# Kernel optimization log

Hardware: AMD Instinct MI355X
Metric: run time of the kernel (lower is better)

## Reference

```python
import jax, jax.numpy as jnp
import numpy as np

N_NODES = 100_000
N_EDGES = 1_600_000
N_TOKENS = 16
VOCAB = 32_000
TOK_DIM = 64
NODE_DIM = 64
HID = 128
FC = 128
NUM_GRAPHS = 1024


def setup_inputs() -> dict:
    key = jax.random.key(0)
    ks = jax.random.split(key, 14)
    emb = jax.random.normal(ks[0], (VOCAB, TOK_DIM), jnp.float32) * 0.02
    emb = emb.at[0].set(0.0)  # padding_idx=0 row is zero
    return {
        "x_token_idxs": jax.random.randint(ks[1], (N_NODES, N_TOKENS), 0, VOCAB),
        "edge_index": jax.random.randint(ks[2], (2, N_EDGES), 0, N_NODES),
        "batch": jnp.sort(jax.random.randint(ks[3], (N_NODES,), 0, NUM_GRAPHS)),
        "emb": emb,
        "Wp": jax.random.normal(ks[4], (TOK_DIM, NODE_DIM), jnp.float32) * (1.0 / np.sqrt(TOK_DIM)),
        "bp": jnp.zeros((NODE_DIM,), jnp.float32),
        "W1": jax.random.normal(ks[5], (NODE_DIM, HID), jnp.float32) * (1.0 / np.sqrt(NODE_DIM)),
        "b1": jnp.zeros((HID,), jnp.float32),
        "W2": jax.random.normal(ks[6], (HID, HID), jnp.float32) * (1.0 / np.sqrt(HID)),
        "b2": jnp.zeros((HID,), jnp.float32),
        "Wfc": jax.random.normal(ks[7], (HID, FC), jnp.float32) * (1.0 / np.sqrt(HID)),
        "bfc": jnp.zeros((FC,), jnp.float32),
        "Wout": jax.random.normal(ks[8], (FC, 1), jnp.float32) * (1.0 / np.sqrt(FC)),
        "bout": jnp.zeros((1,), jnp.float32),
    }


def reference(x_token_idxs, edge_index, batch, emb, Wp, bp, W1, b1, W2, b2, Wfc, bfc, Wout, bout):
    N = x_token_idxs.shape[0]
    # token embed -> mean pool over tokens -> node projection
    node = emb[x_token_idxs].mean(axis=1) @ Wp + bp  # [N, NODE_DIM]

    # GCN normalization with self-loops (PyG gcn_norm, symmetric)
    loops = jnp.arange(N)
    src = jnp.concatenate([edge_index[0], loops])
    dst = jnp.concatenate([edge_index[1], loops])
    deg = jax.ops.segment_sum(jnp.ones_like(dst, jnp.float32), dst, num_segments=N)
    dis = jnp.where(deg > 0, jax.lax.rsqrt(deg), 0.0)
    norm = (dis[src] * dis[dst])[:, None]  # [E+N, 1]

    def gcn(x, W, b):
        h = x @ W                                      # linear transform first (in->out)
        msg = h[src] * norm                            # gather + scale
        return jax.ops.segment_sum(msg, dst, num_segments=N) + b  # scatter-add + bias

    x = jax.nn.relu(gcn(node, W1, b1))
    x = jax.nn.relu(gcn(x, W2, b2))

    # global mean pool by graph id
    cnt = jax.ops.segment_sum(jnp.ones((N,), jnp.float32), batch, num_segments=NUM_GRAPHS)
    g = jax.ops.segment_sum(x, batch, num_segments=NUM_GRAPHS) / jnp.maximum(cnt, 1.0)[:, None]

    g = jax.nn.relu(g @ Wfc + bfc)
    logits = (g @ Wout + bout).squeeze(-1)  # [NUM_GRAPHS]
    return jax.nn.sigmoid(logits), logits
```

## Files before the change

kernel.cpp:

```cpp
#include <hip/hip_runtime.h>
#include <hip/hip_bf16.h>
#include <hip/hip_fp16.h>
#include <math.h>

#define N_TOKENS 16
#define TOK_DIM 64
#define NODE_DIM 64
#define HID 128
#define FC 128
#define NUM_GRAPHS 1024
#define NBUCK_MAX 512
#define CHUNK 8192

typedef _Float16 f16x8 __attribute__((ext_vector_type(8)));
typedef float f32x4 __attribute__((ext_vector_type(4)));

__device__ __forceinline__ __half2 shfl_xor_h2(__half2 v, int mask) {
    int i = *(int*)&v;
    i = __shfl_xor(i, mask);
    return *(__half2*)&i;
}

__global__ void prep_weights_kernel(const float* __restrict__ Wp, const float* __restrict__ W1,
                                    const float* __restrict__ W2, const float* __restrict__ bp,
                                    _Float16* __restrict__ Wf16t, _Float16* __restrict__ W2t,
                                    float* __restrict__ bf) {
    int n = blockIdx.x;
    int t = threadIdx.x;
    if (t < 64) {
        float acc = 0.f;
#pragma unroll
        for (int d = 0; d < 64; d++) acc += Wp[t * 64 + d] * W1[d * 128 + n];
        Wf16t[(size_t)n * 64 + t] = (_Float16)acc;
    } else {
        int d = t - 64;
        float v = bp[d] * W1[d * 128 + n];
#pragma unroll
        for (int off = 32; off > 0; off >>= 1) v += __shfl_down(v, off);
        if (d == 0) bf[n] = v;
    }
    W2t[(size_t)n * 128 + t] = (_Float16)W2[(size_t)t * 128 + n];
}

__global__ void embed_mean_kernel(const int* __restrict__ tok,
                                  const float* __restrict__ emb,
                                  __half* __restrict__ mean16, int N) {
    int t = threadIdx.x;
    int w = t >> 6, j = t & 63;
    int q = j >> 4, l = j & 15;
    int i = blockIdx.x * 4 + w;
    if (i >= N) return;
    const float4* e4 = (const float4*)emb;
    int t0 = tok[i * 16 + q];
    int t1 = tok[i * 16 + q + 4];
    int t2 = tok[i * 16 + q + 8];
    int t3 = tok[i * 16 + q + 12];
    float4 v0 = e4[(size_t)t0 * 16 + l];
    float4 v1 = e4[(size_t)t1 * 16 + l];
    float4 v2 = e4[(size_t)t2 * 16 + l];
    float4 v3 = e4[(size_t)t3 * 16 + l];
    float4 s;
    s.x = v0.x + v1.x + v2.x + v3.x;
    s.y = v0.y + v1.y + v2.y + v3.y;
    s.z = v0.z + v1.z + v2.z + v3.z;
    s.w = v0.w + v1.w + v2.w + v3.w;
    s.x += __shfl_xor(s.x, 16); s.y += __shfl_xor(s.y, 16);
    s.z += __shfl_xor(s.z, 16); s.w += __shfl_xor(s.w, 16);
    s.x += __shfl_xor(s.x, 32); s.y += __shfl_xor(s.y, 32);
    s.z += __shfl_xor(s.z, 32); s.w += __shfl_xor(s.w, 32);
    if (q == 0) {
        const float inv = 1.0f / 16.0f;
        __half2 h0 = __floats2half2_rn(s.x * inv, s.y * inv);
        __half2 h1 = __floats2half2_rn(s.z * inv, s.w * inv);
        float2 packed;
        ((__half2*)&packed)[0] = h0;
        ((__half2*)&packed)[1] = h1;
        ((float2*)mean16)[(size_t)i * 16 + l] = packed;
    }
}

__global__ void bucket_hist_kernel(const int* __restrict__ dst, int* __restrict__ bucket_cnt,
                                   int E, int nbuck) {
    __shared__ int h[NBUCK_MAX];
    int t = threadIdx.x;
    for (int i = t; i < nbuck; i += 256) h[i] = 0;
    __syncthreads();
    int base = blockIdx.x * CHUNK;
    for (int i = t; i < CHUNK; i += 256) {
        int e = base + i;
        if (e < E) atomicAdd(&h[dst[e] >> 8], 1);
    }
    __syncthreads();
    for (int i = t; i < nbuck; i += 256)
        if (h[i]) atomicAdd(&bucket_cnt[i], h[i]);
}

__global__ void bucket_scan_kernel(const int* __restrict__ bucket_cnt,
                                   int* __restrict__ bucket_base,
                                   int* __restrict__ bucket_cursor, int nbuck) {
    __shared__ int s[512];
    int tid = threadIdx.x;
    int v = (tid < nbuck) ? bucket_cnt[tid] : 0;
    s[tid] = v;
    __syncthreads();
    for (int off = 1; off < 512; off <<= 1) {
        int add = (tid >= off) ? s[tid - off] : 0;
        __syncthreads();
        s[tid] += add;
        __syncthreads();
    }
    if (tid < nbuck) { bucket_base[tid] = s[tid] - v; bucket_cursor[tid] = 0; }
    if (tid == 511) bucket_base[nbuck] = s[511];
}

__global__ void binscatter_kernel(const int* __restrict__ src, const int* __restrict__ dst,
                                  const int* __restrict__ bucket_base,
                                  int* __restrict__ bucket_cursor,
                                  int* __restrict__ staged, int E, int nbuck) {
    __shared__ int h[NBUCK_MAX];
    __shared__ int gw[NBUCK_MAX];
    int t = threadIdx.x;
    for (int i = t; i < nbuck; i += 256) h[i] = 0;
    __syncthreads();
    int base = blockIdx.x * CHUNK;
    for (int i = t; i < CHUNK; i += 256) {
        int e = base + i;
        if (e < E) atomicAdd(&h[dst[e] >> 8], 1);
    }
    __syncthreads();
    for (int i = t; i < nbuck; i += 256) {
        int c = h[i];
        gw[i] = (c > 0) ? bucket_base[i] + atomicAdd(&bucket_cursor[i], c) : 0;
        h[i] = 0;
    }
    __syncthreads();
    for (int i = t; i < CHUNK; i += 256) {
        int e = base + i;
        if (e < E) {
            int d = dst[e], s = src[e];
            int b = d >> 8;
            int r = atomicAdd(&h[b], 1);
            staged[gw[b] + r] = s | ((d & 255) << 17);
        }
    }
}

__global__ void bucket_count_kernel(const int* __restrict__ staged,
                                    const int* __restrict__ bucket_base,
                                    int* __restrict__ row_start, float* __restrict__ dis,
                                    int N, int E) {
    __shared__ int cnt[256];
    __shared__ int sc[256];
    int b = blockIdx.x;
    int t = threadIdx.x;
    cnt[t] = 0;
    __syncthreads();
    int rb0 = bucket_base[b], rb1 = bucket_base[b + 1];
    for (int i = rb0 + t; i < rb1; i += 256) atomicAdd(&cnt[staged[i] >> 17], 1);
    __syncthreads();
    int v = cnt[t];
    sc[t] = v;
    __syncthreads();
    for (int off = 1; off < 256; off <<= 1) {
        int add = (t >= off) ? sc[t - off] : 0;
        __syncthreads();
        sc[t] += add;
        __syncthreads();
    }
    int node = b * 256 + t;
    if (node < N) {
        row_start[node] = rb0 + sc[t] - v;
        dis[node] = rsqrtf(1.0f + (float)v);
    }
    if (b == 0 && t == 0) row_start[N] = E;
}

__global__ void csr_write_kernel(const int* __restrict__ staged,
                                 const int* __restrict__ bucket_base,
                                 const int* __restrict__ row_start,
                                 const float* __restrict__ dis,
                                 int2* __restrict__ csr, float* __restrict__ rowsum, int N) {
    __shared__ int cur[256];
    __shared__ float dl[256];
    __shared__ float wsum[256];
    int b = blockIdx.x;
    int t = threadIdx.x;
    int node = b * 256 + t;
    cur[t] = (node < N) ? row_start[node] : 0;
    dl[t] = (node < N) ? dis[node] : 0.f;
    wsum[t] = 0.f;
    __syncthreads();
    int rb0 = bucket_base[b], rb1 = bucket_base[b + 1];
    for (int i = rb0 + t; i < rb1; i += 256) {
        int v = staged[i];
        int s = v & 131071;
        int dloc = v >> 17;
        float w = dis[s] * dl[dloc];
        int pos = atomicAdd(&cur[dloc], 1);
        __half2 wh = __floats2half2_rn(w, w);
        csr[pos] = make_int2(s, *(int*)&wh);
        atomicAdd(&wsum[dloc], w);
    }
    __syncthreads();
    if (node < N) rowsum[node] = wsum[t] + dl[t] * dl[t];
}

__global__ __launch_bounds__(256, 8)
void agg64_kernel(const __half* __restrict__ mean16,
                  const int* __restrict__ row_start,
                  const int2* __restrict__ csr,
                  const float* __restrict__ dis,
                  __half* __restrict__ agg16, int N) {
    int t = threadIdx.x;
    int w = t >> 6, j = t & 63;
    int q = j >> 3, l = j & 7;
    int node = blockIdx.x * 4 + w;
    if (node >= N) return;
    int beg = row_start[node];
    int end = row_start[node + 1];
    float d = dis[node];
    const float4* m4 = (const float4*)mean16;
    __half2 a0, a1, a2, a3;
    {
        float4 raw = m4[(size_t)node * 8 + l];
        const __half2* hp = (const __half2*)&raw;
        float d2f = d * d * ((q == 0) ? 1.f : 0.f);
        __half2 d2h = __floats2half2_rn(d2f, d2f);
        a0 = __hmul2(hp[0], d2h); a1 = __hmul2(hp[1], d2h);
        a2 = __hmul2(hp[2], d2h); a3 = __hmul2(hp[3], d2h);
    }
    int k = beg;
    int kfull = beg + ((end - beg) & ~31);
    for (; k < kfull; k += 32) {
        int2 e[4];
        float4 v[4];
#pragma unroll
        for (int m = 0; m < 4; m++) e[m] = csr[k + 8 * m + q];
#pragma unroll
        for (int m = 0; m < 4; m++) v[m] = m4[(size_t)e[m].x * 8 + l];
#pragma unroll
        for (int m = 0; m < 4; m++) {
            __half2 wh = *(__half2*)&e[m].y;
            const __half2* hp = (const __half2*)&v[m];
            a0 = __hfma2(hp[0], wh, a0);
            a1 = __hfma2(hp[1], wh, a1);
            a2 = __hfma2(hp[2], wh, a2);
            a3 = __hfma2(hp[3], wh, a3);
        }
    }
    for (; k < end; k += 16) {
        int2 e[2];
        float4 v[2];
#pragma unroll
        for (int m = 0; m < 2; m++) {
            int kk = k + 8 * m + q;
            e[m] = (kk < end) ? csr[kk] : make_int2(0, 0);
        }
#pragma unroll
        for (int m = 0; m < 2; m++) v[m] = m4[(size_t)e[m].x * 8 + l];
#pragma unroll
        for (int m = 0; m < 2; m++) {
            __half2 wh = *(__half2*)&e[m].y;
            const __half2* hp = (const __half2*)&v[m];
            a0 = __hfma2(hp[0], wh, a0);
            a1 = __hfma2(hp[1], wh, a1);
            a2 = __hfma2(hp[2], wh, a2);
            a3 = __hfma2(hp[3], wh, a3);
        }
    }
#pragma unroll
    for (int mask = 8; mask <= 32; mask <<= 1) {
        a0 = __hadd2(a0, shfl_xor_h2(a0, mask));
        a1 = __hadd2(a1, shfl_xor_h2(a1, mask));
        a2 = __hadd2(a2, shfl_xor_h2(a2, mask));
        a3 = __hadd2(a3, shfl_xor_h2(a3, mask));
    }
    if (q == 0) {
        float4 packed;
        __half2* pp = (__half2*)&packed;
        pp[0] = a0; pp[1] = a1; pp[2] = a2; pp[3] = a3;
        ((float4*)agg16)[(size_t)node * 8 + l] = packed;
    }
}

#define NB 32
__global__ void dense_chain_mfma_kernel(const __half* __restrict__ agg16,
                                        const float* __restrict__ rowsum,
                                        const _Float16* __restrict__ Wf16t,
                                        const float* __restrict__ bf,
                                        const float* __restrict__ b1,
                                        const _Float16* __restrict__ W2t,
                                        __half* __restrict__ h2, int N) {
    __shared__ _Float16 sx1[32][136];
    __shared__ float srs[32];
    int t = threadIdx.x;
    int wv = t >> 6, lane = t & 63;
    int nb0 = blockIdx.x * NB;
    int rh = wv & 1;
    int ncb = (wv >> 1) * 64;
    int m16 = lane & 15;
    int q = lane >> 4;

    if (t < 32) srs[t] = (nb0 + t < N) ? rowsum[nb0 + t] : 0.f;

    f32x4 c0 = {}, c1 = {}, c2 = {}, c3 = {};
    int arow = nb0 + rh * 16 + m16;
    bool rowok = (arow < N);
    const _Float16* ag = (const _Float16*)agg16;
#pragma unroll
    for (int ks = 0; ks < 2; ks++) {
        int k0 = ks * 32 + q * 8;
        f16x8 afrag = {};
        if (rowok) afrag = *(const f16x8*)(ag + (size_t)arow * 64 + k0);
        f16x8 b0 = *(const f16x8*)(Wf16t + (size_t)(ncb + 0 * 16 + m16) * 64 + k0);
        f16x8 b1f = *(const f16x8*)(Wf16t + (size_t)(ncb + 1 * 16 + m16) * 64 + k0);
        f16x8 b2f = *(const f16x8*)(Wf16t + (size_t)(ncb + 2 * 16 + m16) * 64 + k0);
        f16x8 b3f = *(const f16x8*)(Wf16t + (size_t)(ncb + 3 * 16 + m16) * 64 + k0);
        c0 = __builtin_amdgcn_mfma_f32_16x16x32_f16(afrag, b0, c0, 0, 0, 0);
        c1 = __builtin_amdgcn_mfma_f32_16x16x32_f16(afrag, b1f, c1, 0, 0, 0);
        c2 = __builtin_amdgcn_mfma_f32_16x16x32_f16(afrag, b2f, c2, 0, 0, 0);
        c3 = __builtin_amdgcn_mfma_f32_16x16x32_f16(afrag, b3f, c3, 0, 0, 0);
    }
    __syncthreads();
    {
        f32x4 cc[4] = {c0, c1, c2, c3};
#pragma unroll
        for (int nt = 0; nt < 4; nt++) {
            int ncol = ncb + nt * 16 + m16;
            float bfj = bf[ncol], b1j = b1[ncol];
#pragma unroll
            for (int r = 0; r < 4; r++) {
                int mrow = q * 4 + r;
                float z = cc[nt][r] + srs[rh * 16 + mrow] * bfj + b1j;
                sx1[rh * 16 + mrow][ncol] = (_Float16)fmaxf(z, 0.f);
            }
        }
    }
    __syncthreads();

    f32x4 d0 = {}, d1 = {}, d2 = {}, d3 = {};
#pragma unroll
    for (int ks = 0; ks < 4; ks++) {
        int k0 = ks * 32 + q * 8;
        f16x8 afrag = *(const f16x8*)(&sx1[rh * 16 + m16][k0]);
        f16x8 b0 = *(const f16x8*)(W2t + (size_t)(ncb + 0 * 16 + m16) * 128 + k0);
        f16x8 b1f = *(const f16x8*)(W2t + (size_t)(ncb + 1 * 16 + m16) * 128 + k0);
        f16x8 b2f = *(const f16x8*)(W2t + (size_t)(ncb + 2 * 16 + m16) * 128 + k0);
        f16x8 b3f = *(const f16x8*)(W2t + (size_t)(ncb + 3 * 16 + m16) * 128 + k0);
        d0 = __builtin_amdgcn_mfma_f32_16x16x32_f16(afrag, b0, d0, 0, 0, 0);
        d1 = __builtin_amdgcn_mfma_f32_16x16x32_f16(afrag, b1f, d1, 0, 0, 0);
        d2 = __builtin_amdgcn_mfma_f32_16x16x32_f16(afrag, b2f, d2, 0, 0, 0);
        d3 = __builtin_amdgcn_mfma_f32_16x16x32_f16(afrag, b3f, d3, 0, 0, 0);
    }
    {
        f32x4 dd[4] = {d0, d1, d2, d3};
#pragma unroll
        for (int nt = 0; nt < 4; nt++) {
            int ncol = ncb + nt * 16 + m16;
#pragma unroll
            for (int r = 0; r < 4; r++) {
                int node = nb0 + rh * 16 + q * 4 + r;
                if (node < N) h2[(size_t)node * 128 + ncol] = __float2half(dd[nt][r]);
            }
        }
    }
}

__global__ __launch_bounds__(256, 8)
void gcn_agg128_kernel(const __half* __restrict__ hsrc,
                       const int* __restrict__ row_start,
                       const int2* __restrict__ csr,
                       const float* __restrict__ dis,
                       const float* __restrict__ b2,
                       __half* __restrict__ outx, int N) {
    int t = threadIdx.x;
    int w = t >> 6, j = t & 63;
    int q = j >> 4, l = j & 15;
    int node = blockIdx.x * 4 + w;
    if (node >= N) return;
    const float4* h4 = (const float4*)hsrc;
    int beg = row_start[node];
    int end = row_start[node + 1];
    float d = dis[node];
    __half2 a0, a1, a2, a3;
    {
        float4 raw = h4[(size_t)node * 16 + l];
        const __half2* hp = (const __half2*)&raw;
        float d2f = d * d * ((q == 0) ? 1.f : 0.f);
        __half2 d2h = __floats2half2_rn(d2f, d2f);
        a0 = __hmul2(hp[0], d2h); a1 = __hmul2(hp[1], d2h);
        a2 = __hmul2(hp[2], d2h); a3 = __hmul2(hp[3], d2h);
    }
    int k = beg;
    int kfull = beg + ((end - beg) & ~31);
    for (; k < kfull; k += 32) {
        int2 e[8];
        float4 v[8];
#pragma unroll
        for (int m = 0; m < 8; m++) e[m] = csr[k + 4 * m + q];
#pragma unroll
        for (int m = 0; m < 8; m++) v[m] = h4[(size_t)e[m].x * 16 + l];
#pragma unroll
        for (int m = 0; m < 8; m++) {
            __half2 wh = *(__half2*)&e[m].y;
            const __half2* hp = (const __half2*)&v[m];
            a0 = __hfma2(hp[0], wh, a0);
            a1 = __hfma2(hp[1], wh, a1);
            a2 = __hfma2(hp[2], wh, a2);
            a3 = __hfma2(hp[3], wh, a3);
        }
    }
    for (; k < end; k += 16) {
        int2 e[4];
        float4 v[4];
#pragma unroll
        for (int m = 0; m < 4; m++) {
            int kk = k + 4 * m + q;
            e[m] = (kk < end) ? csr[kk] : make_int2(0, 0);
        }
#pragma unroll
        for (int m = 0; m < 4; m++) v[m] = h4[(size_t)e[m].x * 16 + l];
#pragma unroll
        for (int m = 0; m < 4; m++) {
            __half2 wh = *(__half2*)&e[m].y;
            const __half2* hp = (const __half2*)&v[m];
            a0 = __hfma2(hp[0], wh, a0);
            a1 = __hfma2(hp[1], wh, a1);
            a2 = __hfma2(hp[2], wh, a2);
            a3 = __hfma2(hp[3], wh, a3);
        }
    }
#pragma unroll
    for (int mask = 16; mask <= 32; mask <<= 1) {
        a0 = __hadd2(a0, shfl_xor_h2(a0, mask));
        a1 = __hadd2(a1, shfl_xor_h2(a1, mask));
        a2 = __hadd2(a2, shfl_xor_h2(a2, mask));
        a3 = __hadd2(a3, shfl_xor_h2(a3, mask));
    }
    if (q == 0) {
        float2 f0 = __half22float2(a0), f1 = __half22float2(a1);
        float2 f2 = __half22float2(a2), f3 = __half22float2(a3);
        const float4* b4 = (const float4*)b2;
        float4 ba = b4[l * 2], bb = b4[l * 2 + 1];
        __half2 o0 = __floats2half2_rn(fmaxf(f0.x + ba.x, 0.f), fmaxf(f0.y + ba.y, 0.f));
        __half2 o1 = __floats2half2_rn(fmaxf(f1.x + ba.z, 0.f), fmaxf(f1.y + ba.w, 0.f));
        __half2 o2 = __floats2half2_rn(fmaxf(f2.x + bb.x, 0.f), fmaxf(f2.y + bb.y, 0.f));
        __half2 o3 = __floats2half2_rn(fmaxf(f3.x + bb.z, 0.f), fmaxf(f3.y + bb.w, 0.f));
        float4 packed;
        __half2* pp = (__half2*)&packed;
        pp[0] = o0; pp[1] = o1; pp[2] = o2; pp[3] = o3;
        ((float4*)outx)[(size_t)node * 16 + l] = packed;
    }
}

__device__ __forceinline__ int lower_bound_i(const int* __restrict__ a, int n, int val) {
    int lo = 0, hi = n;
    while (lo < hi) {
        int mid = (lo + hi) >> 1;
        if (a[mid] < val) lo = mid + 1; else hi = mid;
    }
    return lo;
}

__global__ void pool_head_kernel(const __half* __restrict__ x,
                                 const int* __restrict__ batch,
                                 const float* __restrict__ Wfc,
                                 const float* __restrict__ bfc,
                                 const float* __restrict__ Wout,
                                 const float* __restrict__ bout,
                                 float* __restrict__ out, int N) {
    int gr = blockIdx.x;
    int j = threadIdx.x;
    __shared__ float sg[128];
    __shared__ float sred[128];
    int beg = lower_bound_i(batch, N, gr);
    int end = lower_bound_i(batch, N, gr + 1);
    float acc = 0.f;
    int i = beg;
    for (; i + 4 <= end; i += 4) {
        float v0 = __half2float(x[(size_t)i * 128 + j]);
        float v1 = __half2float(x[(size_t)(i + 1) * 128 + j]);
        float v2 = __half2float(x[(size_t)(i + 2) * 128 + j]);
        float v3 = __half2float(x[(size_t)(i + 3) * 128 + j]);
        acc += v0 + v1 + v2 + v3;
    }
    for (; i < end; i++) acc += __half2float(x[(size_t)i * 128 + j]);
    float cnt = fmaxf((float)(end - beg), 1.0f);
    sg[j] = acc / cnt;
    __syncthreads();
    float a = bfc[j];
#pragma unroll
    for (int k = 0; k < 128; k++) a += sg[k] * Wfc[k * 128 + j];
    float f = fmaxf(a, 0.f);
    sred[j] = f * Wout[j];
    __syncthreads();
    if (j < 64) sred[j] += sred[j + 64];
    __syncthreads();
    if (j < 64) {
        float v = sred[j];
#pragma unroll
        for (int off = 32; off > 0; off >>= 1) v += __shfl_down(v, off);
        if (j == 0) {
            float logit = v + bout[0];
            out[gr] = 1.0f / (1.0f + expf(-logit));
            out[NUM_GRAPHS + gr] = logit;
        }
    }
}

extern "C" void kernel_launch(void* const* d_in, const int* in_sizes, int n_in,
                              void* d_out, int out_size, void* d_ws, size_t ws_size,
                              hipStream_t stream) {
    const int* tok   = (const int*)d_in[0];
    const int* eidx  = (const int*)d_in[1];
    const int* batch = (const int*)d_in[2];
    const float* emb = (const float*)d_in[3];
    const float* Wp  = (const float*)d_in[4];
    const float* bp  = (const float*)d_in[5];
    const float* W1  = (const float*)d_in[6];
    const float* b1  = (const float*)d_in[7];
    const float* W2  = (const float*)d_in[8];
    const float* b2  = (const float*)d_in[9];
    const float* Wfc = (const float*)d_in[10];
    const float* bfc = (const float*)d_in[11];
    const float* Wout= (const float*)d_in[12];
    const float* bout= (const float*)d_in[13];
    float* out = (float*)d_out;

    const int N = in_sizes[2];
    const int E = in_sizes[1] / 2;
    const int* src = eidx;
    const int* dst = eidx + E;
    const int Np = (N + 3) & ~3;
    const int nbuck = (N + 255) / 256;
    const int nchunk = (E + CHUNK - 1) / CHUNK;

    float* ws = (float*)d_ws;
    size_t off = 0;
    float* dis     = ws + off;            off += Np;
    __half* mean16 = (__half*)(ws + off); off += (size_t)Np * 32;
    __half* agg16  = (__half*)(ws + off); off += (size_t)Np * 32;
    float* rowsum  = ws + off;            off += Np;
    __half* h2buf  = (__half*)(ws + off); off += (size_t)Np * 64;
    __half* xfin16 = (__half*)(ws + off); off += (size_t)Np * 64;
    _Float16* Wf16t = (_Float16*)(ws + off); off += 4096;
    _Float16* W2t   = (_Float16*)(ws + off); off += 8192;
    float* bf      = ws + off;            off += 128;
    int* row_start = (int*)(ws + off);    off += Np + 4;
    int* staged    = (int*)(ws + off);    off += E;
    int* bucket_cnt    = (int*)(ws + off); off += NBUCK_MAX;
    int* bucket_base   = (int*)(ws + off); off += NBUCK_MAX + 8;
    int* bucket_cursor = (int*)(ws + off); off += NBUCK_MAX;
    int2* csr      = (int2*)(ws + off);

    prep_weights_kernel<<<128, 128, 0, stream>>>(Wp, W1, W2, bp, Wf16t, W2t, bf);

    hipMemsetAsync(bucket_cnt, 0, nbuck * sizeof(int), stream);
    bucket_hist_kernel<<<nchunk, 256, 0, stream>>>(dst, bucket_cnt, E, nbuck);
    bucket_scan_kernel<<<1, 512, 0, stream>>>(bucket_cnt, bucket_base, bucket_cursor, nbuck);
    binscatter_kernel<<<nchunk, 256, 0, stream>>>(src, dst, bucket_base, bucket_cursor,
                                                  staged, E, nbuck);
    bucket_count_kernel<<<nbuck, 256, 0, stream>>>(staged, bucket_base, row_start, dis, N, E);
    csr_write_kernel<<<nbuck, 256, 0, stream>>>(staged, bucket_base, row_start, dis,
                                                csr, rowsum, N);

    embed_mean_kernel<<<(N + 3) / 4, 256, 0, stream>>>(tok, emb, mean16, N);

    agg64_kernel<<<(N + 3) / 4, 256, 0, stream>>>(mean16, row_start, csr, dis, agg16, N);

    dense_chain_mfma_kernel<<<(N + NB - 1) / NB, 256, 0, stream>>>(agg16, rowsum, Wf16t,
                                                                   bf, b1, W2t, h2buf, N);

    gcn_agg128_kernel<<<(N + 3) / 4, 256, 0, stream>>>(h2buf, row_start, csr, dis, b2,
                                                       xfin16, N);

    pool_head_kernel<<<NUM_GRAPHS, 128, 0, stream>>>(xfin16, batch, Wfc, bfc, Wout, bout,
                                                     out, N);
}
```

Baseline: 360.1 us.

## Gather fp16 embeddings, widen bucket blocks, vectorize pooling reads

Converts the fp32 embedding table to fp16 once per call and gathers half-width rows in the token-mean kernel, summing with half2 adds. This halves the random-gather traffic over the 6.4M token lookups, at the cost of an extra conversion pass and lower-precision accumulation of 16 values. It also raises the histogram and binscatter block size to 512 threads, and rewrites the pool head to read half2 pairs split across two waves.

```diff
diff --git a/kernel.cpp b/kernel.cpp
--- a/kernel.cpp
+++ b/kernel.cpp
@@ -42,40 +42,55 @@
     W2t[(size_t)n * 128 + t] = (_Float16)W2[(size_t)t * 128 + n];
 }
 
+__global__ void convert_emb_kernel(const float* __restrict__ emb, __half* __restrict__ emb16,
+                                   int n4) {
+    int i = blockIdx.x * 256 + threadIdx.x;
+    if (i < n4) {
+        float4 v = ((const float4*)emb)[i];
+        __half2 h0 = __floats2half2_rn(v.x, v.y);
+        __half2 h1 = __floats2half2_rn(v.z, v.w);
+        float2 p;
+        ((__half2*)&p)[0] = h0;
+        ((__half2*)&p)[1] = h1;
+        ((float2*)emb16)[i] = p;
+    }
+}
+
 __global__ void embed_mean_kernel(const int* __restrict__ tok,
-                                  const float* __restrict__ emb,
+                                  const __half* __restrict__ emb16,
                                   __half* __restrict__ mean16, int N) {
     int t = threadIdx.x;
     int w = t >> 6, j = t & 63;
-    int q = j >> 4, l = j & 15;
+    int q = j >> 3, l = j & 7;
     int i = blockIdx.x * 4 + w;
     if (i >= N) return;
-    const float4* e4 = (const float4*)emb;
+    const float4* e4 = (const float4*)emb16;
     int t0 = tok[i * 16 + q];
-    int t1 = tok[i * 16 + q + 4];
-    int t2 = tok[i * 16 + q + 8];
-    int t3 = tok[i * 16 + q + 12];
-    float4 v0 = e4[(size_t)t0 * 16 + l];
-    float4 v1 = e4[(size_t)t1 * 16 + l];
-    float4 v2 = e4[(size_t)t2 * 16 + l];
-    float4 v3 = e4[(size_t)t3 * 16 + l];
-    float4 s;
-    s.x = v0.x + v1.x + v2.x + v3.x;
-    s.y = v0.y + v1.y + v2.y + v3.y;
-    s.z = v0.z + v1.z + v2.z + v3.z;
-    s.w = v0.w + v1.w + v2.w + v3.w;
-    s.x += __shfl_xor(s.x, 16); s.y += __shfl_xor(s.y, 16);
-    s.z += __shfl_xor(s.z, 16); s.w += __shfl_xor(s.w, 16);
-    s.x += __shfl_xor(s.x, 32); s.y += __shfl_xor(s.y, 32);
-    s.z += __shfl_xor(s.z, 32); s.w += __shfl_xor(s.w, 32);
+    int t1 = tok[i * 16 + q + 8];
+    float4 v0 = e4[(size_t)t0 * 8 + l];
+    float4 v1 = e4[(size_t)t1 * 8 + l];
+    const __half2* p0 = (const __half2*)&v0;
+    const __half2* p1 = (const __half2*)&v1;
+    __half2 a0 = __hadd2(p0[0], p1[0]);
+    __half2 a1 = __hadd2(p0[1], p1[1]);
+    __half2 a2 = __hadd2(p0[2], p1[2]);
+    __half2 a3 = __hadd2(p0[3], p1[3]);
+#pragma unroll
+    for (int mask = 8; mask <= 32; mask <<= 1) {
+        a0 = __hadd2(a0, shfl_xor_h2(a0, mask));
+        a1 = __hadd2(a1, shfl_xor_h2(a1, mask));
+        a2 = __hadd2(a2, shfl_xor_h2(a2, mask));
+        a3 = __hadd2(a3, shfl_xor_h2(a3, mask));
+    }
     if (q == 0) {
-        const float inv = 1.0f / 16.0f;
-        __half2 h0 = __floats2half2_rn(s.x * inv, s.y * inv);
-        __half2 h1 = __floats2half2_rn(s.z * inv, s.w * inv);
-        float2 packed;
-        ((__half2*)&packed)[0] = h0;
-        ((__half2*)&packed)[1] = h1;
-        ((float2*)mean16)[(size_t)i * 16 + l] = packed;
+        __half2 inv = __floats2half2_rn(1.0f / 16.0f, 1.0f / 16.0f);
+        float4 packed;
+        __half2* pp = (__half2*)&packed;
+        pp[0] = __hmul2(a0, inv);
+        pp[1] = __hmul2(a1, inv);
+        pp[2] = __hmul2(a2, inv);
+        pp[3] = __hmul2(a3, inv);
+        ((float4*)mean16)[(size_t)i * 8 + l] = packed;
     }
 }
 
@@ -83,15 +98,15 @@
                                    int E, int nbuck) {
     __shared__ int h[NBUCK_MAX];
     int t = threadIdx.x;
-    for (int i = t; i < nbuck; i += 256) h[i] = 0;
+    for (int i = t; i < nbuck; i += 512) h[i] = 0;
     __syncthreads();
     int base = blockIdx.x * CHUNK;
-    for (int i = t; i < CHUNK; i += 256) {
+    for (int i = t; i < CHUNK; i += 512) {
         int e = base + i;
         if (e < E) atomicAdd(&h[dst[e] >> 8], 1);
     }
     __syncthreads();
-    for (int i = t; i < nbuck; i += 256)
+    for (int i = t; i < nbuck; i += 512)
         if (h[i]) atomicAdd(&bucket_cnt[i], h[i]);
 }
 
@@ -120,21 +135,21 @@
     __shared__ int h[NBUCK_MAX];
     __shared__ int gw[NBUCK_MAX];
     int t = threadIdx.x;
-    for (int i = t; i < nbuck; i += 256) h[i] = 0;
+    for (int i = t; i < nbuck; i += 512) h[i] = 0;
     __syncthreads();
     int base = blockIdx.x * CHUNK;
-    for (int i = t; i < CHUNK; i += 256) {
+    for (int i = t; i < CHUNK; i += 512) {
         int e = base + i;
         if (e < E) atomicAdd(&h[dst[e] >> 8], 1);
     }
     __syncthreads();
-    for (int i = t; i < nbuck; i += 256) {
+    for (int i = t; i < nbuck; i += 512) {
         int c = h[i];
         gw[i] = (c > 0) ? bucket_base[i] + atomicAdd(&bucket_cursor[i], c) : 0;
         h[i] = 0;
     }
     __syncthreads();
-    for (int i = t; i < CHUNK; i += 256) {
+    for (int i = t; i < CHUNK; i += 512) {
         int e = base + i;
         if (e < E) {
             int d = dst[e], s = src[e];
@@ -470,24 +485,29 @@
                                  const float* __restrict__ bout,
                                  float* __restrict__ out, int N) {
     int gr = blockIdx.x;
-    int j = threadIdx.x;
+    int t = threadIdx.x;
+    int j2 = t & 63, w = t >> 6;
+    __shared__ float2 spart[2][64];
     __shared__ float sg[128];
     __shared__ float sred[128];
     int beg = lower_bound_i(batch, N, gr);
     int end = lower_bound_i(batch, N, gr + 1);
-    float acc = 0.f;
-    int i = beg;
-    for (; i + 4 <= end; i += 4) {
-        float v0 = __half2float(x[(size_t)i * 128 + j]);
-        float v1 = __half2float(x[(size_t)(i + 1) * 128 + j]);
-        float v2 = __half2float(x[(size_t)(i + 2) * 128 + j]);
-        float v3 = __half2float(x[(size_t)(i + 3) * 128 + j]);
-        acc += v0 + v1 + v2 + v3;
-    }
-    for (; i < end; i++) acc += __half2float(x[(size_t)i * 128 + j]);
-    float cnt = fmaxf((float)(end - beg), 1.0f);
-    sg[j] = acc / cnt;
-    __syncthreads();
+    const __half2* x2 = (const __half2*)x;
+    float2 acc = make_float2(0.f, 0.f);
+    for (int i = beg + w; i < end; i += 2) {
+        float2 a = __half22float2(x2[(size_t)i * 64 + j2]);
+        acc.x += a.x; acc.y += a.y;
+    }
+    spart[w][j2] = acc;
+    __syncthreads();
+    if (t < 64) {
+        float inv = 1.0f / fmaxf((float)(end - beg), 1.0f);
+        float2 s0 = spart[0][t], s1 = spart[1][t];
+        sg[2 * t] = (s0.x + s1.x) * inv;
+        sg[2 * t + 1] = (s0.y + s1.y) * inv;
+    }
+    __syncthreads();
+    int j = t;
     float a = bfc[j];
 #pragma unroll
     for (int k = 0; k < 128; k++) a += sg[k] * Wfc[k * 128 + j];
@@ -534,6 +554,7 @@
     const int Np = (N + 3) & ~3;
     const int nbuck = (N + 255) / 256;
     const int nchunk = (E + CHUNK - 1) / CHUNK;
+    const int emb_n4 = in_sizes[3] / 4;
 
     float* ws = (float*)d_ws;
     size_t off = 0;
@@ -543,6 +564,7 @@
     float* rowsum  = ws + off;            off += Np;
     __half* h2buf  = (__half*)(ws + off); off += (size_t)Np * 64;
     __half* xfin16 = (__half*)(ws + off); off += (size_t)Np * 64;
+    __half* emb16  = (__half*)(ws + off); off += (size_t)(in_sizes[3] / 2 + 4);
     _Float16* Wf16t = (_Float16*)(ws + off); off += 4096;
     _Float16* W2t   = (_Float16*)(ws + off); off += 8192;
     float* bf      = ws + off;            off += 128;
@@ -554,17 +576,18 @@
     int2* csr      = (int2*)(ws + off);
 
     prep_weights_kernel<<<128, 128, 0, stream>>>(Wp, W1, W2, bp, Wf16t, W2t, bf);
+    convert_emb_kernel<<<(emb_n4 + 255) / 256, 256, 0, stream>>>(emb, emb16, emb_n4);
 
     hipMemsetAsync(bucket_cnt, 0, nbuck * sizeof(int), stream);
-    bucket_hist_kernel<<<nchunk, 256, 0, stream>>>(dst, bucket_cnt, E, nbuck);
+    bucket_hist_kernel<<<nchunk, 512, 0, stream>>>(dst, bucket_cnt, E, nbuck);
     bucket_scan_kernel<<<1, 512, 0, stream>>>(bucket_cnt, bucket_base, bucket_cursor, nbuck);
-    binscatter_kernel<<<nchunk, 256, 0, stream>>>(src, dst, bucket_base, bucket_cursor,
+    binscatter_kernel<<<nchunk, 512, 0, stream>>>(src, dst, bucket_base, bucket_cursor,
                                                   staged, E, nbuck);
     bucket_count_kernel<<<nbuck, 256, 0, stream>>>(staged, bucket_base, row_start, dis, N, E);
     csr_write_kernel<<<nbuck, 256, 0, stream>>>(staged, bucket_base, row_start, dis,
                                                 csr, rowsum, N);
 
-    embed_mean_kernel<<<(N + 3) / 4, 256, 0, stream>>>(tok, emb, mean16, N);
+    embed_mean_kernel<<<(N + 3) / 4, 256, 0, stream>>>(tok, emb16, mean16, N);
 
     agg64_kernel<<<(N + 3) / 4, 256, 0, stream>>>(mean16, row_start, csr, dis, agg16, N);
 
```

Measured after the change: 347.3 us, median of 2. 3.6% less time.
